# Kernel optimization log

Measured on AMD Instinct MI355X. Metric: run time of the kernel, lower is better.

Reference implementation:

```python
import jax, jax.numpy as jnp
import numpy as np

LOSS_WEIGHT = 1.0


def _similarity_transform(S1, S2):
    """Align S1 (K,3) to S2 (K,3) with a scaled rigid (Procrustes/Kabsch) transform.

    Mirrors compute_similarity_transform_torch(target[i], output[i]).
    """
    mu1 = jnp.mean(S1, axis=0, keepdims=True)  # (1,3)
    mu2 = jnp.mean(S2, axis=0, keepdims=True)
    X1 = S1 - mu1
    X2 = S2 - mu2
    var1 = jnp.sum(X1 * X1)
    K = X1.T @ X2  # (3,3) cross-covariance
    U, s, Vh = jnp.linalg.svd(K)
    # reflection fix: det(R) must be +1
    detsign = jnp.sign(jnp.linalg.det(U @ Vh))
    Z = jnp.diag(jnp.stack([jnp.ones((), S1.dtype), jnp.ones((), S1.dtype), detsign]))
    R = Vh.T @ Z @ U.T  # (3,3) optimal rotation
    scale = jnp.trace(R @ K) / var1
    t = mu2 - scale * (mu1 @ R.T)  # (1,3)
    return scale * (S1 @ R.T) + t  # (K,3) aligned


def setup_inputs() -> dict:
    key = jax.random.key(0)
    k1, k2 = jax.random.split(key)
    N, K, D = 65536, 133, 3
    output = jax.random.normal(k1, (N, K, D), dtype=jnp.float32)
    target = jax.random.normal(k2, (N, K, D), dtype=jnp.float32)
    return {"output": output, "target": target}


def reference(output, target):
    # batched Procrustes alignment of each target sample onto its output sample
    target_aligned = jax.vmap(_similarity_transform)(target, output)  # (N,K,3)
    loss = jnp.mean(jnp.linalg.norm(output - target_aligned, axis=-1))
    return loss * LOSS_WEIGHT
```

## Files before the change

kernel.cpp:

```cpp
#include <hip/hip_runtime.h>
#include <hip/hip_fp16.h>
#include <math.h>

#define KPTS 133
#define FPS  (KPTS * 3)
#define SPB  16
#define SPWV 4

#define DPP_XOR1(x) __int_as_float(__builtin_amdgcn_update_dpp(0, __float_as_int(x), 0xB1, 0xF, 0xF, true))
#define DPP_XOR2(x) __int_as_float(__builtin_amdgcn_update_dpp(0, __float_as_int(x), 0x4E, 0xF, 0xF, true))

#define PINU(x) asm volatile("" : "+v"(x))

__device__ __forceinline__ float2 f2(float a, float b) { return make_float2(a, b); }

__device__ __forceinline__ unsigned pack2h(float a, float b) {
    __half2 h = __float22half2_rn(make_float2(a, b));
    union { __half2 h; unsigned u; } c; c.h = h; return c.u;
}
__device__ __forceinline__ float2 unpack2h(unsigned u) {
    union { unsigned u; __half2 h; } c; c.u = u;
    return make_float2(__half2float(__low2half(c.h)), __half2float(__high2half(c.h)));
}

__device__ __forceinline__ float det3(float a0, float a1, float a2,
                                      float b0, float b1, float b2,
                                      float c0, float c1, float c2) {
    return a0 * (b1 * c2 - b2 * c1)
         - a1 * (b0 * c2 - b2 * c0)
         + a2 * (b0 * c1 - b1 * c0);
}

__global__ __launch_bounds__(256, 4) void pa_mpjpe_kernel(
    const float* __restrict__ outp,
    const float* __restrict__ tgtp,
    float* __restrict__ block_sums,
    int nsamp)
{
    const int tid  = threadIdx.x;
    const int lane = tid & 63;
    const int wid  = tid >> 6;
    const int l16  = lane & 15;
    const int s_l  = wid * SPWV + (lane >> 4);
    int s = blockIdx.x * SPB + s_l;
    const bool valid = (s < nsamp);
    if (!valid) s = 0;

    __shared__ float momT[SPB][17];
    __shared__ float prm[SPB][13];
    __shared__ float shs[SPB];

    const float3* tb3 = reinterpret_cast<const float3*>(tgtp + (size_t)s * FPS);
    const float3* ob3 = reinterpret_cast<const float3*>(outp + (size_t)s * FPS);

    float2 P0 = f2(0,0), P1 = f2(0,0), P2 = f2(0,0), P3 = f2(0,0);
    float2 P4 = f2(0,0), P5 = f2(0,0), P6 = f2(0,0), P7 = f2(0,0);
    float2 Q  = f2(0,0);

#define DECLPT(k) unsigned uT_##k = 0u, uM_##k = 0u, uO_##k = 0u;
#define LOADACC(k, P) {                                                     \
    const float3 t = tb3[(P)];                                              \
    const float3 o = ob3[(P)];                                              \
    P0 += f2(t.x, t.y);                                                     \
    P1 += f2(t.z, o.x);                                                     \
    P2 += f2(o.y, o.z);                                                     \
    P3 += f2(t.x, t.x) * f2(o.x, o.y);                                      \
    P4 += f2(t.x, t.y) * f2(o.z, o.x);                                      \
    P5 += f2(t.y, t.y) * f2(o.y, o.z);                                      \
    P6 += f2(t.z, t.z) * f2(o.x, o.y);                                      \
    P7 += f2(t.z, t.x) * f2(o.z, t.x);                                      \
    Q  += f2(t.y, t.z) * f2(t.y, t.z);                                      \
    uT_##k = pack2h(t.x, t.y);                                              \
    uM_##k = pack2h(t.z, o.x);                                              \
    uO_##k = pack2h(o.y, o.z);                                              \
}
#define PINPT(k) PINU(uT_##k); PINU(uM_##k); PINU(uO_##k);

    DECLPT(0) DECLPT(1) DECLPT(2) DECLPT(3)
    DECLPT(4) DECLPT(5) DECLPT(6) DECLPT(7)
    DECLPT(8)

    LOADACC(0, l16 +   0)
    LOADACC(1, l16 +  16)
    LOADACC(2, l16 +  32)
    LOADACC(3, l16 +  48)
    LOADACC(4, l16 +  64)
    LOADACC(5, l16 +  80)
    LOADACC(6, l16 +  96)
    LOADACC(7, l16 + 112)
    if (l16 < 5) {
        LOADACC(8, 128 + l16)
    }

    PINPT(0) PINPT(1) PINPT(2) PINPT(3)
    PINPT(4) PINPT(5) PINPT(6) PINPT(7)
    PINPT(8)

    float red[16];
    red[0]  = P0.x; red[1]  = P0.y; red[2]  = P1.x; red[3]  = P1.y;
    red[4]  = P2.x; red[5]  = P2.y; red[6]  = P3.x; red[7]  = P3.y;
    red[8]  = P4.x; red[9]  = P4.y; red[10] = P5.x; red[11] = P5.y;
    red[12] = P6.x; red[13] = P6.y; red[14] = P7.x; red[15] = P7.y + Q.x + Q.y;

    float v8[8];
    {
        const bool b = (lane & 1);
        #pragma unroll
        for (int m = 0; m < 8; ++m) {
            const float snd = b ? red[2 * m] : red[2 * m + 1];
            const float rcv = DPP_XOR1(snd);
            v8[m] = (b ? red[2 * m + 1] : red[2 * m]) + rcv;
        }
    }
    float v4_[4];
    {
        const bool b = ((lane >> 1) & 1);
        #pragma unroll
        for (int m = 0; m < 4; ++m) {
            const float snd = b ? v8[2 * m] : v8[2 * m + 1];
            const float rcv = DPP_XOR2(snd);
            v4_[m] = (b ? v8[2 * m + 1] : v8[2 * m]) + rcv;
        }
    }
    float v2_[2];
    {
        const bool b = ((lane >> 2) & 1);
        #pragma unroll
        for (int m = 0; m < 2; ++m) {
            const float snd = b ? v4_[2 * m] : v4_[2 * m + 1];
            const float rcv = __shfl_xor(snd, 4, 64);
            v2_[m] = (b ? v4_[2 * m + 1] : v4_[2 * m]) + rcv;
        }
    }
    float v1;
    {
        const bool b = ((lane >> 3) & 1);
        const float snd = b ? v2_[0] : v2_[1];
        const float rcv = __shfl_xor(snd, 8, 64);
        v1 = (b ? v2_[1] : v2_[0]) + rcv;
    }

    momT[s_l][l16] = v1;
    __syncthreads();

    if (wid == 0 && lane < SPB && (blockIdx.x * SPB + lane) < nsamp) {
        float m_[16];
        #pragma unroll
        for (int j = 0; j < 16; ++j) m_[j] = momT[lane][j];

        const float invK = 1.0f / (float)KPTS;
        const float mu1x = m_[0] * invK, mu1y = m_[1] * invK, mu1z = m_[2] * invK;
        const float mu2x = m_[3] * invK, mu2y = m_[4] * invK, mu2z = m_[5] * invK;

        const float Sxx = m_[6]  - m_[0] * m_[3] * invK;
        const float Sxy = m_[7]  - m_[0] * m_[4] * invK;
        const float Sxz = m_[8]  - m_[0] * m_[5] * invK;
        const float Syx = m_[9]  - m_[1] * m_[3] * invK;
        const float Syy = m_[10] - m_[1] * m_[4] * invK;
        const float Syz = m_[11] - m_[1] * m_[5] * invK;
        const float Szx = m_[12] - m_[2] * m_[3] * invK;
        const float Szy = m_[13] - m_[2] * m_[4] * invK;
        const float Szz = m_[14] - m_[2] * m_[5] * invK;
        const float var1 = m_[15] - (m_[0] * m_[0] + m_[1] * m_[1] + m_[2] * m_[2]) * invK;

        const float N00 = Sxx + Syy + Szz;
        const float N01 = Syz - Szy, N02 = Szx - Sxz, N03 = Sxy - Syx;
        const float N11 = Sxx - Syy - Szz, N12 = Sxy + Syx, N13 = Szx + Sxz;
        const float N22 = -Sxx + Syy - Szz, N23 = Syz + Szy;
        const float N33 = -Sxx - Syy + Szz;

        const float trKtK = Sxx * Sxx + Sxy * Sxy + Sxz * Sxz
                          + Syx * Syx + Syy * Syy + Syz * Syz
                          + Szx * Szx + Szy * Szy + Szz * Szz;
        const float c2 = -2.0f * trKtK;
        const float detK = det3(Sxx, Sxy, Sxz, Syx, Syy, Syz, Szx, Szy, Szz);
        const float c1 = -8.0f * detK;
        const float c0 =
              N00 * det3(N11, N12, N13, N12, N22, N23, N13, N23, N33)
            - N01 * det3(N01, N12, N13, N02, N22, N23, N03, N23, N33)
            + N02 * det3(N01, N11, N13, N02, N12, N23, N03, N13, N33)
            - N03 * det3(N01, N11, N12, N02, N12, N22, N03, N13, N23);

        float lam = sqrtf(fmaxf(3.0f * trKtK, 0.0f));
        #pragma unroll
        for (int it = 0; it < 10; ++it) {
            const float l2 = lam * lam;
            const float P  = (l2 + c2) * l2 + c1 * lam + c0;
            const float Pp = (4.0f * l2 + 2.0f * c2) * lam + c1;
            lam -= P / Pp;
        }

        const float M00 = N00 - lam, M11 = N11 - lam, M22 = N22 - lam, M33 = N33 - lam;
        const float a0 =  det3(M11, N12, N13, N12, M22, N23, N13, N23, M33);
        const float a1 = -det3(N01, N12, N13, N02, M22, N23, N03, N23, M33);
        const float a2 =  det3(N01, M11, N13, N02, N12, N23, N03, N13, M33);
        const float a3 = -det3(N01, M11, N12, N02, N12, M22, N03, N13, N23);
        const float b0 = -det3(N01, N02, N03, N12, M22, N23, N13, N23, M33);
        const float b1 =  det3(M00, N02, N03, N02, M22, N23, N03, N23, M33);
        const float b2 = -det3(M00, N01, N03, N02, N12, N23, N03, N13, M33);
        const float b3 =  det3(M00, N01, N02, N02, N12, M22, N03, N13, N23);
        const float na = a0 * a0 + a1 * a1 + a2 * a2 + a3 * a3;
        const float nb = b0 * b0 + b1 * b1 + b2 * b2 + b3 * b3;
        const bool pa_ = (na >= nb);
        float qw = pa_ ? a0 : b0;
        float qx = pa_ ? a1 : b1;
        float qy = pa_ ? a2 : b2;
        float qz = pa_ ? a3 : b3;
        const float qn = rsqrtf(fmaxf(qw * qw + qx * qx + qy * qy + qz * qz, 1e-30f));
        qw *= qn; qx *= qn; qy *= qn; qz *= qn;

        const float R00 = 1.0f - 2.0f * (qy * qy + qz * qz);
        const float R01 = 2.0f * (qx * qy - qw * qz);
        const float R02 = 2.0f * (qx * qz + qw * qy);
        const float R10 = 2.0f * (qx * qy + qw * qz);
        const float R11 = 1.0f - 2.0f * (qx * qx + qz * qz);
        const float R12 = 2.0f * (qy * qz - qw * qx);
        const float R20 = 2.0f * (qx * qz - qw * qy);
        const float R21 = 2.0f * (qy * qz + qw * qx);
        const float R22 = 1.0f - 2.0f * (qx * qx + qy * qy);

        const float trRK = R00 * Sxx + R01 * Syx + R02 * Szx
                         + R10 * Sxy + R11 * Syy + R12 * Szy
                         + R20 * Sxz + R21 * Syz + R22 * Szz;
        const float scale = trRK / var1;

        const float tx = mu2x - scale * (R00 * mu1x + R01 * mu1y + R02 * mu1z);
        const float ty = mu2y - scale * (R10 * mu1x + R11 * mu1y + R12 * mu1z);
        const float tz = mu2z - scale * (R20 * mu1x + R21 * mu1y + R22 * mu1z);

        prm[lane][0] = scale * R00; prm[lane][1] = scale * R01; prm[lane][2] = scale * R02;
        prm[lane][3] = scale * R10; prm[lane][4] = scale * R11; prm[lane][5] = scale * R12;
        prm[lane][6] = scale * R20; prm[lane][7] = scale * R21; prm[lane][8] = scale * R22;
        prm[lane][9] = tx; prm[lane][10] = ty; prm[lane][11] = tz;
    }
    __syncthreads();

    const float2 rA = f2(prm[s_l][0], prm[s_l][3]);
    const float2 rB = f2(prm[s_l][1], prm[s_l][4]);
    const float2 rC = f2(prm[s_l][2], prm[s_l][5]);
    const float sR20 = prm[s_l][6], sR21 = prm[s_l][7], sR22 = prm[s_l][8];
    const float2 txy = f2(prm[s_l][9], prm[s_l][10]);
    const float tz = prm[s_l][11];

    float rsum = 0.0f;
#define RESPT(k)                                                            \
    {                                                                       \
        const float2 pT = unpack2h(uT_##k);                     \
        const float2 pM = unpack2h(uM_##k);                     \
        const float2 pO = unpack2h(uO_##k);                     \
        float2 axy = txy;                                                   \
        axy += rA * f2(pT.x, pT.x);                                         \
        axy += rB * f2(pT.y, pT.y);                                         \
        axy += rC * f2(pM.x, pM.x);                                         \
        const float az = fmaf(sR20, pT.x, fmaf(sR21, pT.y, fmaf(sR22, pM.x, tz))); \
        const float2 dxy = f2(pM.y, pO.x) - axy;                            \
        const float dz = pO.y - az;                                         \
        const float ns = fmaf(dxy.x, dxy.x, fmaf(dxy.y, dxy.y, dz * dz));   \
        rsum += sqrtf(ns);                                                  \
    }

    RESPT(0) RESPT(1) RESPT(2) RESPT(3)
    RESPT(4) RESPT(5) RESPT(6) RESPT(7)
    if (l16 < 5) { RESPT(8) }

    rsum = valid ? rsum : 0.0f;

    rsum += DPP_XOR1(rsum);
    rsum += DPP_XOR2(rsum);
    rsum += __shfl_xor(rsum, 4, 64);
    rsum += __shfl_xor(rsum, 8, 64);

    if (l16 == 0) shs[s_l] = rsum;
    __syncthreads();
    if (tid == 0) {
        float b = 0.0f;
        #pragma unroll
        for (int i = 0; i < SPB; ++i) b += shs[i];
        block_sums[blockIdx.x] = b;
    }
}

__global__ __launch_bounds__(256) void pa_reduce_kernel(
    const float* __restrict__ block_sums, int n,
    float* __restrict__ out, float inv_total)
{
    __shared__ float sh[4];
    float a0 = 0.f, a1 = 0.f, a2 = 0.f, a3 = 0.f;
    for (int i = (int)threadIdx.x * 4; i < n; i += 1024) {
        if (i + 0 < n) a0 += block_sums[i + 0];
        if (i + 1 < n) a1 += block_sums[i + 1];
        if (i + 2 < n) a2 += block_sums[i + 2];
        if (i + 3 < n) a3 += block_sums[i + 3];
    }
    float v = (a0 + a1) + (a2 + a3);
    #pragma unroll
    for (int off = 32; off >= 1; off >>= 1) v += __shfl_xor(v, off, 64);
    const int lane = threadIdx.x & 63;
    const int wid  = threadIdx.x >> 6;
    if (lane == 0) sh[wid] = v;
    __syncthreads();
    if (threadIdx.x == 0) out[0] = (sh[0] + sh[1] + sh[2] + sh[3]) * inv_total;
}

extern "C" void kernel_launch(void* const* d_in, const int* in_sizes, int n_in,
                              void* d_out, int out_size, void* d_ws, size_t ws_size,
                              hipStream_t stream) {
    const float* outp = (const float*)d_in[0];
    const float* tgtp = (const float*)d_in[1];
    const int nsamp   = in_sizes[0] / FPS;
    const int nblocks = (nsamp + SPB - 1) / SPB;

    float* bsums = (float*)d_ws;

    pa_mpjpe_kernel<<<nblocks, 256, 0, stream>>>(outp, tgtp, bsums, nsamp);
    pa_reduce_kernel<<<1, 256, 0, stream>>>(
        bsums, nblocks, (float*)d_out,
        1.0f / ((float)nsamp * (float)KPTS));
}
```

Baseline: 41.47 us.

## Assign 32 lanes per sample instead of 16 to halve per-thread keypoints

Each sample is now processed by 32 lanes instead of 16, so each thread loads and stores about 5 keypoints rather than 9, and each block covers 8 samples instead of 16. An extra xor-16 shuffle stage is added to both the moment reduction and the residual reduction. The aim is fewer live registers per thread and more memory-level parallelism. The cost is twice as many blocks, more partial block sums, and a lane of 16 that sits partly idle on the 5-point tail.

```diff
diff --git a/kernel.cpp b/kernel.cpp
--- a/kernel.cpp
+++ b/kernel.cpp
@@ -4,8 +4,8 @@
 
 #define KPTS 133
 #define FPS  (KPTS * 3)
-#define SPB  16
-#define SPWV 4
+#define SPB  8
+#define SPWV 2
 
 #define DPP_XOR1(x) __int_as_float(__builtin_amdgcn_update_dpp(0, __float_as_int(x), 0xB1, 0xF, 0xF, true))
 #define DPP_XOR2(x) __int_as_float(__builtin_amdgcn_update_dpp(0, __float_as_int(x), 0x4E, 0xF, 0xF, true))
@@ -40,8 +40,9 @@
     const int tid  = threadIdx.x;
     const int lane = tid & 63;
     const int wid  = tid >> 6;
+    const int l32  = lane & 31;
     const int l16  = lane & 15;
-    const int s_l  = wid * SPWV + (lane >> 4);
+    const int s_l  = wid * SPWV + (lane >> 5);
     int s = blockIdx.x * SPB + s_l;
     const bool valid = (s < nsamp);
     if (!valid) s = 0;
@@ -76,25 +77,17 @@
 }
 #define PINPT(k) PINU(uT_##k); PINU(uM_##k); PINU(uO_##k);
 
-    DECLPT(0) DECLPT(1) DECLPT(2) DECLPT(3)
-    DECLPT(4) DECLPT(5) DECLPT(6) DECLPT(7)
-    DECLPT(8)
-
-    LOADACC(0, l16 +   0)
-    LOADACC(1, l16 +  16)
-    LOADACC(2, l16 +  32)
-    LOADACC(3, l16 +  48)
-    LOADACC(4, l16 +  64)
-    LOADACC(5, l16 +  80)
-    LOADACC(6, l16 +  96)
-    LOADACC(7, l16 + 112)
-    if (l16 < 5) {
-        LOADACC(8, 128 + l16)
-    }
-
-    PINPT(0) PINPT(1) PINPT(2) PINPT(3)
-    PINPT(4) PINPT(5) PINPT(6) PINPT(7)
-    PINPT(8)
+    DECLPT(0) DECLPT(1) DECLPT(2) DECLPT(3) DECLPT(4)
+
+    LOADACC(0, l32 +  0)
+    LOADACC(1, l32 + 32)
+    LOADACC(2, l32 + 64)
+    LOADACC(3, l32 + 96)
+    if (l32 < 5) {
+        LOADACC(4, 128 + l32)
+    }
+
+    PINPT(0) PINPT(1) PINPT(2) PINPT(3) PINPT(4)
 
     float red[16];
     red[0]  = P0.x; red[1]  = P0.y; red[2]  = P1.x; red[3]  = P1.y;
@@ -139,8 +132,9 @@
         const float rcv = __shfl_xor(snd, 8, 64);
         v1 = (b ? v2_[1] : v2_[0]) + rcv;
     }
-
-    momT[s_l][l16] = v1;
+    v1 += __shfl_xor(v1, 16, 64);
+
+    if (l32 < 16) momT[s_l][l16] = v1;
     __syncthreads();
 
     if (wid == 0 && lane < SPB && (blockIdx.x * SPB + lane) < nsamp) {
@@ -260,8 +254,7 @@
     }
 
     RESPT(0) RESPT(1) RESPT(2) RESPT(3)
-    RESPT(4) RESPT(5) RESPT(6) RESPT(7)
-    if (l16 < 5) { RESPT(8) }
+    if (l32 < 5) { RESPT(4) }
 
     rsum = valid ? rsum : 0.0f;
 
@@ -269,8 +262,9 @@
     rsum += DPP_XOR2(rsum);
     rsum += __shfl_xor(rsum, 4, 64);
     rsum += __shfl_xor(rsum, 8, 64);
-
-    if (l16 == 0) shs[s_l] = rsum;
+    rsum += __shfl_xor(rsum, 16, 64);
+
+    if (l32 == 0) shs[s_l] = rsum;
     __syncthreads();
     if (tid == 0) {
         float b = 0.0f;
```

After: 48.66 us. +17.3%, slower.
